# Optimization experiments

Hardware: AMD Instinct MI355X
Metric: run time of the kernel (lower is better)

## Reference

```python
import jax, jax.numpy as jnp
import numpy as np
from jax import lax

T, B, C = 50, 50, 4096
PADLEN = 49
ORDER = 2
BANDS = [(0.05, 0.15), (0.2, 0.4)]


def _butter_bandpass_sos(n, w1, w2):
    """Butterworth bandpass design (scipy.signal.iirfilter(..., ftype='butter', output='sos') equivalent)."""
    fs = 2.0
    warped = 2.0 * fs * np.tan(np.pi * np.array([w1, w2]) / fs)  # pre-warped analog freqs
    bw = warped[1] - warped[0]
    wo = np.sqrt(warped[0] * warped[1])
    k = np.arange(1, n + 1)
    p = -np.exp(1j * np.pi * (2 * k - 1) / (2 * n))  # analog LP prototype poles
    # lp2bp: n poles -> 2n poles, n zeros at origin, gain *= bw**n
    p_lp = p * bw / 2.0
    disc = np.sqrt(p_lp ** 2 - wo ** 2 + 0j)
    p_bp = np.concatenate([p_lp + disc, p_lp - disc])
    # bilinear transform (fs=2): zeros at origin -> +1; n zeros at infinity -> -1
    fs2 = 2.0 * fs
    p_d = (fs2 + p_bp) / (fs2 - p_bp)
    gain = (bw ** n) * (fs2 ** n) / np.real(np.prod(fs2 - p_bp))
    # pair conjugate poles into biquads; numerator (z-1)(z+1) = [1, 0, -1]
    pos = p_d[np.imag(p_d) > 0]
    assert len(pos) == n, 'expected complex-conjugate pole pairs'
    sos = []
    for i, pp in enumerate(pos):
        a = np.array([1.0, -2.0 * np.real(pp), np.abs(pp) ** 2])
        b = np.array([1.0, 0.0, -1.0])
        if i == 0:
            b = b * gain
        sos.append(np.concatenate([b, a]))
    return np.array(sos)  # [n_sections, 6]


def _sosfilt_zi(sos):
    """scipy.signal.sosfilt_zi: steady-state per-section initial conditions (DF2T)."""
    n_sections = sos.shape[0]
    zi = np.zeros((n_sections, 2))
    scale = 1.0
    for s in range(n_sections):
        b, a = sos[s, :3], sos[s, 3:]
        B0 = b[1] - a[1] * b[0]
        B1 = b[2] - a[2] * b[0]
        det = 1.0 + a[1] + a[2]
        zi[s, 0] = scale * (B0 + B1) / det
        zi[s, 1] = scale * ((1.0 + a[1]) * B1 - a[2] * B0) / det
        scale *= b.sum() / a.sum()
    return zi


def _sosfilt(sos, x, zi):
    """Cascaded biquads, direct form II transposed, scan over time axis 0.
    x: [T, B, C]; zi: list of (z0, z1) each [B, C]."""
    y = x
    for s in range(sos.shape[0]):
        b0, b1, b2 = (float(sos[s, 0]), float(sos[s, 1]), float(sos[s, 2]))
        a1, a2 = float(sos[s, 4]), float(sos[s, 5])
        def step(carry, xt, b0=b0, b1=b1, b2=b2, a1=a1, a2=a2):
            z0, z1 = carry
            yt = b0 * xt + z0
            return (b1 * xt + z1 - a1 * yt, b2 * xt - a2 * yt), yt
        _, y = lax.scan(step, (zi[s][0], zi[s][1]), y)
    return y


def _odd_ext(x, n):
    left = 2.0 * x[0] - x[n:0:-1]
    right = 2.0 * x[-1] - x[-2:-n - 2:-1]
    return jnp.concatenate([left, x, right], axis=0)


def _sosfiltfilt(sos, x, padlen):
    zi = _sosfilt_zi(sos)  # [S, 2] numpy
    ext = _odd_ext(x, padlen)  # [T + 2*padlen, B, C]
    x0 = ext[0]
    zi_f = [(float(zi[s, 0]) * x0, float(zi[s, 1]) * x0) for s in range(sos.shape[0])]
    y = _sosfilt(sos, ext, zi_f)
    y = y[::-1]
    y0 = y[0]
    zi_b = [(float(zi[s, 0]) * y0, float(zi[s, 1]) * y0) for s in range(sos.shape[0])]
    y = _sosfilt(sos, y, zi_b)
    y = y[::-1]
    return y[padlen:-padlen]


def _tensor_zscore(x):
    # Faithful to the original expand([50,-1,-1]).permute(1,0,2) quirk:
    # mean/std over axis 0 give [B, C]; the permute aligns them with the TIME axis,
    # i.e. out[t, b, c] = (x[t, b, c] - m[t, c]) / s[t, c]  (valid since T == B == 50).
    m = x.mean(axis=0)
    s = x.std(axis=0, ddof=1)  # torch.std default is unbiased
    return (x - m[:, None, :]) / s[:, None, :]


def setup_inputs() -> dict:
    key = jax.random.key(0)
    sample = jax.random.normal(key, (T, B, C), dtype=jnp.float32)
    return {"sample": sample}


def reference(sample):
    outs = []
    for (w1, w2) in BANDS:
        sos = _butter_bandpass_sos(ORDER, w1, w2)
        y = _sosfiltfilt(sos, sample, PADLEN)
        y = y - y.mean(axis=0)  # bandpass branch: mean-center
        y = _tensor_zscore(y)   # normalize=True
        outs.append(y)
    return jnp.stack(outs)  # [n_bands, T, B, C]
```

## Files before the change

kernel.cpp:

```cpp
#include <hip/hip_runtime.h>
#include <hip/hip_bf16.h>
#include <cmath>
#include <complex>

constexpr int TT  = 50;
constexpr int NB  = 50;
constexpr int NC  = 4096;
constexpr int NCH = NB * NC;
constexpr int PAD = 49;
constexpr int EXT = TT + 2 * PAD;
constexpr int CT  = 16;

struct Coefs {
    double b0[2][2], b1[2][2], b2[2][2], a1[2][2], a2[2][2];
    double zi0[2][2], zi1[2][2];
};

__global__ void __launch_bounds__(64, 1) build_M(float* __restrict__ Mt, Coefs cf) {
    __shared__ float ylds[EXT][TT];
    const int band = blockIdx.x;
    const int j = threadIdx.x;
    if (j >= TT) return;

    const double b00 = cf.b0[band][0], b10 = cf.b1[band][0], b20 = cf.b2[band][0];
    const double a10 = cf.a1[band][0], a20 = cf.a2[band][0];
    const double b01 = cf.b0[band][1], b11 = cf.b1[band][1], b21 = cf.b2[band][1];
    const double a11 = cf.a1[band][1], a21 = cf.a2[band][1];

    const double x0 = 2.0 * (j == 0 ? 1.0 : 0.0) - (j == PAD ? 1.0 : 0.0);

    double s00 = cf.zi0[band][0] * x0, s01 = cf.zi1[band][0] * x0;
    double s10 = cf.zi0[band][1] * x0, s11 = cf.zi1[band][1] * x0;
    double ylast = 0.0;
#pragma unroll
    for (int i = 0; i < EXT; ++i) {
        double xt;
        if (i < PAD)            xt = 2.0 * (j == 0 ? 1.0 : 0.0) - (j == PAD - i ? 1.0 : 0.0);
        else if (i < PAD + TT)  xt = (j == i - PAD) ? 1.0 : 0.0;
        else                    xt = 2.0 * (j == TT - 1 ? 1.0 : 0.0)
                                     - (j == 2 * TT - 2 - (i - PAD) ? 1.0 : 0.0);
        const double y0 = b00 * xt + s00;
        s00 = b10 * xt + s01 - a10 * y0;
        s01 = b20 * xt - a20 * y0;
        const double y1 = b01 * y0 + s10;
        s10 = b11 * y0 + s11 - a11 * y1;
        s11 = b21 * y0 - a21 * y1;
        ylds[i][j] = (float)y1;
        if (i == EXT - 1) ylast = y1;
    }

    s00 = cf.zi0[band][0] * ylast; s01 = cf.zi1[band][0] * ylast;
    s10 = cf.zi0[band][1] * ylast; s11 = cf.zi1[band][1] * ylast;
    float o[TT];
#pragma unroll
    for (int m = 0; m < EXT; ++m) {
        const int i = EXT - 1 - m;
        const double xt = (double)ylds[i][j];
        const double y0 = b00 * xt + s00;
        s00 = b10 * xt + s01 - a10 * y0;
        s01 = b20 * xt - a20 * y0;
        const double y1 = b01 * y0 + s10;
        s10 = b11 * y0 + s11 - a11 * y1;
        s11 = b21 * y0 - a21 * y1;
        if (i >= PAD && i < PAD + TT) o[i - PAD] = (float)y1;
    }

    float mean = 0.f;
#pragma unroll
    for (int t = 0; t < TT; ++t) mean += o[t];
    mean *= (1.0f / TT);
#pragma unroll
    for (int t = 0; t < TT; ++t)
        Mt[(band * TT + j) * TT + t] = o[t] - mean;
}

__global__ void __launch_bounds__(CT * NB, 3)
filt_main(const float* __restrict__ x, const float* __restrict__ Mt,
          float* __restrict__ out) {
    const int tx = threadIdx.x;
    const int b  = threadIdx.y;
    const int c  = blockIdx.x * CT + tx;
    const int i  = b * NC + c;

    __shared__ float smu[NB][CT], sinv[NB][CT];

#pragma unroll 1
    for (int band = 0; band < 2; ++band) {
        const float* __restrict__ Mb = Mt + band * TT * TT;
        float f[TT];
#pragma unroll
        for (int t = 0; t < TT; ++t) f[t] = 0.f;

#pragma unroll
        for (int k = 0; k < TT; ++k) {
            const float xk = x[(size_t)k * NCH + i];
#pragma unroll
            for (int t = 0; t < TT; ++t) f[t] = fmaf(Mb[k * TT + t], xk, f[t]);
        }

        float mu = 0.f;
#pragma unroll
        for (int t = 0; t < TT; ++t) mu += f[t];
        mu *= (1.0f / TT);
        float ss = 0.f;
#pragma unroll
        for (int t = 0; t < TT; ++t) {
            const float h = f[t] - mu;
            ss = fmaf(h, h, ss);
        }
        smu[b][tx] = mu;
        sinv[b][tx] = 1.0f / sqrtf(ss * (1.0f / (TT - 1)));
        __syncthreads();

#pragma unroll
        for (int t = 0; t < TT; ++t)
            out[(size_t)(band * TT + t) * NCH + i] =
                (f[t] - smu[t][tx]) * sinv[t][tx];
        __syncthreads();
    }
}

static Coefs make_coefs() {
    Coefs cf;
    const double bands[2][2] = {{0.05, 0.15}, {0.2, 0.4}};
    const int n = 2;
    for (int bd = 0; bd < 2; ++bd) {
        const double fs = 2.0;
        const double w1 = bands[bd][0], w2 = bands[bd][1];
        const double warped0 = 2.0 * fs * std::tan(M_PI * w1 / fs);
        const double warped1 = 2.0 * fs * std::tan(M_PI * w2 / fs);
        const double bw = warped1 - warped0;
        const double wo = std::sqrt(warped0 * warped1);
        std::complex<double> p_bp[4];
        for (int k = 1; k <= n; ++k) {
            std::complex<double> p = -std::exp(std::complex<double>(0.0, M_PI * (2 * k - 1) / (2.0 * n)));
            std::complex<double> plp = p * (bw / 2.0);
            std::complex<double> disc = std::sqrt(plp * plp - std::complex<double>(wo * wo, 0.0));
            p_bp[k - 1] = plp + disc;
            p_bp[n + k - 1] = plp - disc;
        }
        const double fs2 = 2.0 * fs;
        std::complex<double> prod(1.0, 0.0);
        for (int i = 0; i < 2 * n; ++i) prod *= (fs2 - p_bp[i]);
        const double gain = std::pow(bw, n) * std::pow(fs2, n) / prod.real();
        std::complex<double> p_d[4];
        for (int i = 0; i < 2 * n; ++i) p_d[i] = (fs2 + p_bp[i]) / (fs2 - p_bp[i]);
        double sos[2][6];
        int cnt = 0;
        for (int i = 0; i < 2 * n; ++i) {
            if (p_d[i].imag() > 0) {
                const double g = (cnt == 0) ? gain : 1.0;
                sos[cnt][0] = g;
                sos[cnt][1] = 0.0;
                sos[cnt][2] = -g;
                sos[cnt][3] = 1.0;
                sos[cnt][4] = -2.0 * p_d[i].real();
                sos[cnt][5] = std::norm(p_d[i]);
                ++cnt;
            }
        }
        double scale = 1.0;
        for (int s = 0; s < 2; ++s) {
            const double b0 = sos[s][0], b1 = sos[s][1], b2 = sos[s][2];
            const double a1 = sos[s][4], a2 = sos[s][5];
            const double B0 = b1 - a1 * b0, B1 = b2 - a2 * b0;
            const double det = 1.0 + a1 + a2;
            cf.b0[bd][s] = b0; cf.b1[bd][s] = b1; cf.b2[bd][s] = b2;
            cf.a1[bd][s] = a1; cf.a2[bd][s] = a2;
            cf.zi0[bd][s] = scale * (B0 + B1) / det;
            cf.zi1[bd][s] = scale * ((1.0 + a1) * B1 - a2 * B0) / det;
            scale *= (b0 + b1 + b2) / (1.0 + a1 + a2);
        }
    }
    return cf;
}

extern "C" void kernel_launch(void* const* d_in, const int* in_sizes, int n_in,
                              void* d_out, int out_size, void* d_ws, size_t ws_size,
                              hipStream_t stream) {
    const float* x = (const float*)d_in[0];
    float* out = (float*)d_out;
    float* Mt = (float*)d_ws;

    const Coefs cf = make_coefs();
    build_M<<<dim3(2), dim3(64), 0, stream>>>(Mt, cf);
    filt_main<<<dim3(NC / CT), dim3(CT, NB), 0, stream>>>(x, Mt, out);
}
```

Measured before the change: 159.8 us.

## Split fused filter kernel into stats pass and recompute output pass

```diff
diff --git a/kernel.cpp b/kernel.cpp
--- a/kernel.cpp
+++ b/kernel.cpp
@@ -9,7 +9,6 @@
 constexpr int NCH = NB * NC;
 constexpr int PAD = 49;
 constexpr int EXT = TT + 2 * PAD;
-constexpr int CT  = 16;
 
 struct Coefs {
     double b0[2][2], b1[2][2], b2[2][2], a1[2][2], a2[2][2];
@@ -74,15 +73,13 @@
         Mt[(band * TT + j) * TT + t] = o[t] - mean;
 }
 
-__global__ void __launch_bounds__(CT * NB, 3)
-filt_main(const float* __restrict__ x, const float* __restrict__ Mt,
-          float* __restrict__ out) {
-    const int tx = threadIdx.x;
-    const int b  = threadIdx.y;
-    const int c  = blockIdx.x * CT + tx;
-    const int i  = b * NC + c;
-
-    __shared__ float smu[NB][CT], sinv[NB][CT];
+__global__ void __launch_bounds__(256)
+stats_k(const float* __restrict__ x, const float* __restrict__ Mt,
+        float2* __restrict__ st) {
+    const int c = blockIdx.x * 64 + threadIdx.x;
+    const int b = blockIdx.y * 4 + threadIdx.y;
+    if (b >= NB) return;
+    const int i = b * NC + c;
 
 #pragma unroll 1
     for (int band = 0; band < 2; ++band) {
@@ -90,14 +87,12 @@
         float f[TT];
 #pragma unroll
         for (int t = 0; t < TT; ++t) f[t] = 0.f;
-
 #pragma unroll
         for (int k = 0; k < TT; ++k) {
             const float xk = x[(size_t)k * NCH + i];
 #pragma unroll
             for (int t = 0; t < TT; ++t) f[t] = fmaf(Mb[k * TT + t], xk, f[t]);
         }
-
         float mu = 0.f;
 #pragma unroll
         for (int t = 0; t < TT; ++t) mu += f[t];
@@ -108,15 +103,36 @@
             const float h = f[t] - mu;
             ss = fmaf(h, h, ss);
         }
-        smu[b][tx] = mu;
-        sinv[b][tx] = 1.0f / sqrtf(ss * (1.0f / (TT - 1)));
-        __syncthreads();
-
-#pragma unroll
-        for (int t = 0; t < TT; ++t)
-            out[(size_t)(band * TT + t) * NCH + i] =
-                (f[t] - smu[t][tx]) * sinv[t][tx];
-        __syncthreads();
+        st[(size_t)(band * NB + b) * NC + c] =
+            make_float2(mu, 1.0f / sqrtf(ss * (1.0f / (TT - 1))));
+    }
+}
+
+__global__ void __launch_bounds__(256)
+out_k(const float* __restrict__ x, const float* __restrict__ Mt,
+      const float2* __restrict__ st, float* __restrict__ out) {
+    const int c = blockIdx.x * 64 + threadIdx.x;
+    const int b = blockIdx.y * 4 + threadIdx.y;
+    if (b >= NB) return;
+    const int i = b * NC + c;
+
+#pragma unroll 1
+    for (int band = 0; band < 2; ++band) {
+        const float* __restrict__ Mb = Mt + band * TT * TT;
+        float f[TT];
+#pragma unroll
+        for (int t = 0; t < TT; ++t) f[t] = 0.f;
+#pragma unroll
+        for (int k = 0; k < TT; ++k) {
+            const float xk = x[(size_t)k * NCH + i];
+#pragma unroll
+            for (int t = 0; t < TT; ++t) f[t] = fmaf(Mb[k * TT + t], xk, f[t]);
+        }
+#pragma unroll
+        for (int t = 0; t < TT; ++t) {
+            const float2 s = st[(size_t)(band * TT + t) * NC + c];
+            out[(size_t)(band * TT + t) * NCH + i] = (f[t] - s.x) * s.y;
+        }
     }
 }
 
@@ -181,8 +197,13 @@
     const float* x = (const float*)d_in[0];
     float* out = (float*)d_out;
     float* Mt = (float*)d_ws;
+    float2* st = (float2*)((char*)d_ws + 32768);
 
     const Coefs cf = make_coefs();
     build_M<<<dim3(2), dim3(64), 0, stream>>>(Mt, cf);
-    filt_main<<<dim3(NC / CT), dim3(CT, NB), 0, stream>>>(x, Mt, out);
-}
+
+    dim3 blk(64, 4);
+    dim3 grd(NC / 64, (NB + 3) / 4);
+    stats_k<<<grd, blk, 0, stream>>>(x, Mt, st);
+    out_k<<<grd, blk, 0, stream>>>(x, Mt, st, out);
+}
```

Result: slower. 203.7 us (+27.5%).
